# Performance work log

Measured on AMD Instinct MI355X. Metric: run time of the kernel, lower is better.

The kernel has to match this reference:

```python
import jax, jax.numpy as jnp
import numpy as np
from math import factorial, sqrt, pi

L = 10  # must match init_kwargs


def setup_inputs() -> dict:
    key = jax.random.key(0)
    pos = jax.random.normal(key, (2_000_000, 3), dtype=jnp.float32)
    return {"pos": pos}


def _cpow_tables(zr, zi, nmax):
    """Powers (zr + i*zi)^n for n=0..nmax. Returns (nmax+1, N) real and imag parts.
    Matches powcmplx in the source (repeated complex multiply), computed once."""
    reals = [jnp.ones_like(zr)]
    imags = [jnp.zeros_like(zr)]
    for _ in range(nmax):
        r, im = reals[-1], imags[-1]
        reals.append(zr * r - zi * im)
        imags.append(zr * im + zi * r)
    return jnp.stack(reals), jnp.stack(imags)


def reference(pos):
    norms = jnp.linalg.norm(pos, axis=1)            # (N,)
    mask = (norms > 0).astype(pos.dtype)            # replaces boolean indexing ids
    x, y, x0 = pos[:, 0], pos[:, 1], pos[:, 2]
    xpl1r, xpl1i = -0.5 * x, -0.5 * y
    xm1r, xm1i = 0.5 * x, -0.5 * y
    # precompute all needed complex powers (same math as powcmplx, deduplicated)
    z1r_t, z1i_t = _cpow_tables(xpl1r, xpl1i, L)    # (L+1, N)
    z2r_t, z2i_t = _cpow_tables(xm1r, xm1i, L)

    clms = [None] * ((L + 1) ** 2)
    i = 0
    for l in range(L + 1):
        rl = norms ** l
        for M in range(-l, 1):
            m = abs(M)
            shr = jnp.zeros_like(x)
            shi = jnp.zeros_like(x)
            for p in range(l + 1):
                q = p - m
                s = l - p - q
                if q >= 0 and s >= 0:
                    z1r, z1i = z1r_t[p], z1i_t[p]
                    z2r, z2i = z2r_t[q], z2i_t[q]
                    # NOTE: faithful to source, including its quirks:
                    # zreal uses z1r**2 - z2i**2, and the term is scaled by x0
                    # (x0**s is computed in the source but never used).
                    zreal = z1r ** 2 - z2i ** 2
                    zimag = z1r * z2i + z1i * z2r
                    c = 1.0 / (factorial(p) * factorial(q) * factorial(s))
                    shr = shr + zreal * x0 * c
                    shi = shi + zimag * x0 * c
            scale = sqrt(factorial(l + m) * factorial(l - m)) * sqrt((2 * l + 1) / (4.0 * pi))
            clm_r = jnp.sum(shr * rl * mask) * scale
            clm_i = jnp.sum(shi * rl * mask) * scale
            if m == 0:
                clms[i] = clm_r
            else:
                f = sqrt(2.0) * (-1) ** m
                clms[i] = f * clm_i
                clms[i + 2 * m] = f * clm_r
            i += 1
        i += l
    return jnp.stack(clms).reshape(-1, 1)  # ((L+1)^2, 1)
```

## Files before the change

### kernel.cpp

```cpp
#include <hip/hip_runtime.h>

namespace {

typedef float v2f __attribute__((ext_vector_type(2)));

constexpr int LMAX  = 10;
constexpr int NPART = 4;
constexpr int PART_OF_L[LMAX + 1] = {3, 2, 1, 0, 1, 2, 3, 3, 2, 1, 0};
constexpr double PI_D = 3.14159265358979323846;

constexpr double dfact(int n) {
    double r = 1.0;
    for (int i = 2; i <= n; ++i) r *= (double)i;
    return r;
}

constexpr double csqrt(double x) {
    if (x <= 0.0) return 0.0;
    double g = x > 1.0 ? x : 1.0;
    for (int i = 0; i < 100; ++i) g = 0.5 * (g + x / g);
    return g;
}

constexpr double FACT[LMAX + 1] = {1., 1., 2., 6., 24., 120., 720., 5040., 40320., 362880., 3628800.};

constexpr int NM_M = 66;
constexpr int mi(int p, int l) { return l * (l + 1) / 2 + p; }
constexpr int ni_base(int l) {
    int c = 0;
    for (int ll = 0; ll < l; ++ll) c += ll / 2;
    return c;
}
constexpr int ni(int q, int l) { return NM_M + ni_base(l) + (q - 1); }
constexpr int NM_N  = 25;
constexpr int NMOM  = NM_M + NM_N;
constexpr int ZSLOT = NMOM;
constexpr int WS_FLOATS = NMOM + 1;

constexpr int part_lmax(int part) {
    int mx = 0;
    for (int l = 0; l <= LMAX; ++l)
        if (PART_OF_L[l] == part) mx = l;
    return mx;
}
constexpr int nls(int part) {
    int c = 0;
    for (int l = 0; l <= LMAX; ++l)
        if (PART_OF_L[l] == part) ++c;
    return c;
}
constexpr int lidx(int part, int l) {
    int c = 0;
    for (int ll = 0; ll < l; ++ll)
        if (PART_OF_L[ll] == part) ++c;
    return c;
}
constexpr int part_ls(int part, int k) {
    int c = 0;
    for (int l = 0; l <= LMAX; ++l)
        if (PART_OF_L[l] == part) {
            if (c == k) return l;
            ++c;
        }
    return -1;
}
constexpr int nM(int part) {
    int c = 0;
    for (int l = 0; l <= LMAX; ++l)
        if (PART_OF_L[l] == part) c += l + 1;
    return c;
}
constexpr int nN(int part) {
    int c = 0;
    for (int l = 0; l <= LMAX; ++l)
        if (PART_OF_L[l] == part) c += l / 2;
    return c;
}
constexpr int nMom(int part) { return nM(part) + nN(part); }
constexpr int nI(int part) {
    int c = 0;
    for (int l = 0; l <= LMAX; ++l)
        if (PART_OF_L[l] == part) c += l;
    return c;
}
constexpr int nAcc(int part) { return nMom(part) + nI(part); }

constexpr int locM(int part, int p, int l) {
    int c = 0;
    for (int ll = 0; ll < l; ++ll)
        if (PART_OF_L[ll] == part) c += ll + 1;
    return c + p;
}
constexpr int locN(int part, int q, int l) {
    int c = nM(part);
    for (int ll = 0; ll < l; ++ll)
        if (PART_OF_L[ll] == part) c += ll / 2;
    return c + (q - 1);
}
constexpr int locI(int part, int m, int l) {
    int c = nMom(part);
    for (int ll = 0; ll < l; ++ll)
        if (PART_OF_L[ll] == part) c += ll;
    return c + (m - 1);
}

constexpr int MAXMOM = 25;
constexpr int MAXIMG = 15;

constexpr float ci_coef(int l, int m, int q) {
    const double c = 1.0 / (FACT[q + m] * FACT[q] * FACT[l - m - 2 * q]);
    return (q & 1) ? (float)(-c) : (float)c;
}

struct PartTab {
    short wsmap[NPART][MAXMOM];
    int   omap[NPART][MAXIMG];
    float oscl[NPART][MAXIMG];
};

constexpr PartTab make_pt() {
    PartTab t{};
    for (int part = 0; part < NPART; ++part) {
        for (int l = 0; l <= LMAX; ++l) {
            if (PART_OF_L[l] != part) continue;
            for (int p = 0; p <= l; ++p) t.wsmap[part][locM(part, p, l)] = (short)mi(p, l);
            for (int q = 1; q <= l / 2; ++q) t.wsmap[part][locN(part, q, l)] = (short)ni(q, l);
            for (int m = 1; m <= l; ++m) {
                const int    k     = locI(part, m, l) - nMom(part);
                const double scale = csqrt(dfact(l + m) * dfact(l - m)) * csqrt((2 * l + 1) / (4.0 * PI_D));
                const double f     = csqrt(2.0) * ((m & 1) ? -1.0 : 1.0);
                const double fold  = ((l - m) <= 1) ? 1.0 / (dfact(m) * dfact(l - m)) : 1.0;
                t.omap[part][k] = l * l + l - m;
                t.oscl[part][k] = (float)(f * scale * fold);
            }
        }
    }
    return t;
}

struct CombTab {
    int   out[66];
    float scale[66];
    int   nt[66];
    float c[66][6];
    short mIx[66][6];
    short nIx[66][6];
};

constexpr CombTab make_comb() {
    CombTab t{};
    int k = 0;
    for (int l = 0; l <= LMAX; ++l) {
        for (int m = 0; m <= l; ++m) {
            const double scale = csqrt(dfact(l + m) * dfact(l - m)) * csqrt((2 * l + 1) / (4.0 * PI_D));
            const double f     = (m == 0) ? 1.0 : csqrt(2.0) * ((m & 1) ? -1.0 : 1.0);
            t.out[k]   = (m == 0) ? l * l + l : l * l + l + m;
            t.scale[k] = (float)(f * scale);
            const int Q = (l - m) / 2;
            t.nt[k]     = Q + 1;
            for (int q = 0; q <= Q; ++q) {
                const double c = 1.0 / (FACT[q + m] * FACT[q] * FACT[l - m - 2 * q]);
                t.c[k][q]   = (float)c;
                t.mIx[k][q] = (short)mi(q + m, l);
                t.nIx[k][q] = (short)(q >= 1 ? ni(q, l) : ZSLOT);
            }
            ++k;
        }
    }
    return t;
}

__constant__ PartTab c_pt = make_pt();
__constant__ CombTab c_cb = make_comb();

__device__ __forceinline__ void pk_fma(v2f& d, v2f a, v2f b) {
    asm("v_pk_fma_f32 %0, %1, %2, %0" : "+v"(d) : "v"(a), "v"(b));
}

__device__ __forceinline__ void load_pair(const float* __restrict__ pos, int ip, int n,
                                          v2f& X, v2f& Y, v2f& Z) {
    const int i0 = 2 * ip;
    if (i0 + 1 < n) {
        const float2* p2 = reinterpret_cast<const float2*>(pos + 3 * i0);
        const float2  a = p2[0], b = p2[1], d = p2[2];
        X.x = a.x; X.y = b.y;
        Y.x = a.y; Y.y = d.x;
        Z.x = b.x; Z.y = d.y;
    } else if (i0 < n) {
        X.x = pos[3 * i0]; Y.x = pos[3 * i0 + 1]; Z.x = pos[3 * i0 + 2];
        X.y = 0.f; Y.y = 0.f; Z.y = 0.f;
    } else {
        X = (v2f)(0.f); Y = (v2f)(0.f); Z = (v2f)(0.f);
    }
}

}

template <int PART>
__device__ __forceinline__ void sht_part(const float* __restrict__ pos, float* __restrict__ out,
                                         float* __restrict__ ws, int n, int nblk) {
    constexpr int PL  = part_lmax(PART);
    constexpr int QX  = PL / 2;
    constexpr int NL  = nls(PART);
    constexpr int NMO = nMom(PART);
    constexpr int NAC = nAcc(PART);

    v2f acc[NAC];
#pragma unroll
    for (int k = 0; k < NAC; ++k) acc[k] = (v2f)(0.f);

    const int bid    = (int)(blockIdx.x >> 2);
    const int tid    = bid * 256 + (int)threadIdx.x;
    const int stride = nblk * 256;
    const int npair  = (n + 1) >> 1;

    v2f X, Y, Z;
    int ip = tid;
    load_pair(pos, ip, n, X, Y, Z);

    while (ip < npair) {
        const int inext = ip + stride;
        v2f       nX, nY, nZ;
        load_pair(pos, inext, n, nX, nY, nZ);

        const v2f r2 = X * X + Y * Y + Z * Z;
        v2f       nrm;
        nrm.x = sqrtf(r2.x);
        nrm.y = sqrtf(r2.y);
        v2f w0;
        w0.x = (nrm.x > 0.f) ? Z.x : 0.f;
        w0.y = (nrm.y > 0.f) ? Z.y : 0.f;

        const v2f ar  = -0.5f * X;
        const v2f ai  = -0.5f * Y;
        const v2f rho = ar * ar + ai * ai;

        v2f wl[NL];
        {
            const v2f p2v = nrm * nrm;
            const v2f p4v = p2v * p2v;
            const v2f p8v = p4v * p4v;
#pragma unroll
            for (int k = 0; k < NL; ++k) {
                const int l = part_ls(PART, k);
                v2f       t = w0;
                if (l & 1) t = t * nrm;
                if (l & 2) t = t * p2v;
                if (l & 4) t = t * p4v;
                if (l & 8) t = t * p8v;
                wl[k] = t;
            }
        }

        v2f zi[PL + 1];
        v2f zrc = (v2f)(1.f), zic = (v2f)(0.f);
#pragma unroll
        for (int p = 0; p <= PL; ++p) {
            if (p) {
                const v2f nr = ar * zrc - ai * zic;
                zic          = ar * zic + ai * zrc;
                zrc          = nr;
            }
            zi[p] = zic;
            const v2f srp = zrc * zrc;
#pragma unroll
            for (int l = 0; l <= LMAX; ++l)
                if (PART_OF_L[l] == PART && l >= p)
                    pk_fma(acc[locM(PART, p, l)], srp, wl[lidx(PART, l)]);
            if (p >= 1 && p <= QX) {
                const v2f sip = zic * zic;
#pragma unroll
                for (int l = 0; l <= LMAX; ++l)
                    if (PART_OF_L[l] == PART && l >= 2 * p)
                        pk_fma(acc[locN(PART, p, l)], sip, wl[lidx(PART, l)]);
            }
        }

#pragma unroll
        for (int l = 0; l <= LMAX; ++l) {
            if (PART_OF_L[l] != PART) continue;
            const v2f wrl = wl[lidx(PART, l)];
#pragma unroll
            for (int m = 1; m <= l; ++m) {
                const int Q = (l - m) >> 1;
                if (Q == 0) {
                    pk_fma(acc[locI(PART, m, l)], zi[m], wrl);
                } else {
                    v2f tq = (v2f)(ci_coef(l, m, Q));
#pragma unroll
                    for (int q = Q - 1; q >= 0; --q) tq = tq * rho + ci_coef(l, m, q);
                    pk_fma(acc[locI(PART, m, l)], tq * zi[m], wrl);
                }
            }
        }

        ip = inext;
        X  = nX;
        Y  = nY;
        Z  = nZ;
    }

    __shared__ float red[4][NAC];
    const int lane = threadIdx.x & 63;
    const int wav  = threadIdx.x >> 6;
#pragma unroll
    for (int k = 0; k < NAC; ++k) {
        float v = acc[k].x + acc[k].y;
#pragma unroll
        for (int off = 32; off > 0; off >>= 1) v += __shfl_down(v, off, 64);
        if (lane == 0) red[wav][k] = v;
    }
    __syncthreads();
    if ((int)threadIdx.x < NAC) {
        const int   k = (int)threadIdx.x;
        const float v = red[0][k] + red[1][k] + red[2][k] + red[3][k];
        if (k < NMO) {
            atomicAdd(&ws[c_pt.wsmap[PART][k]], v);
        } else {
            const int j = k - NMO;
            atomicAdd(&out[c_pt.omap[PART][j]], v * c_pt.oscl[PART][j]);
        }
    }
}

__global__ __launch_bounds__(256, 3) void sht_kernel(const float* __restrict__ pos,
                                                     float* __restrict__ out,
                                                     float* __restrict__ ws, int n, int nblk) {
    switch (blockIdx.x & 3) {
        case 0: sht_part<0>(pos, out, ws, n, nblk); break;
        case 1: sht_part<1>(pos, out, ws, n, nblk); break;
        case 2: sht_part<2>(pos, out, ws, n, nblk); break;
        default: sht_part<3>(pos, out, ws, n, nblk); break;
    }
}

__global__ void sht_combine(const float* __restrict__ ws, float* __restrict__ out) {
    const int t = (int)threadIdx.x;
    if (t < 66) {
        const int nt = c_cb.nt[t];
        float     v  = 0.f;
        for (int j = 0; j < nt; ++j)
            v += c_cb.c[t][j] * (ws[c_cb.mIx[t][j]] - ws[c_cb.nIx[t][j]]);
        out[c_cb.out[t]] = c_cb.scale[t] * v;
    }
}

extern "C" void kernel_launch(void* const* d_in, const int* in_sizes, int n_in,
                              void* d_out, int out_size, void* d_ws, size_t ws_size,
                              hipStream_t stream) {
    const float* pos = (const float*)d_in[0];
    float* out       = (float*)d_out;
    float* ws        = (float*)d_ws;
    const int n      = in_sizes[0] / 3;

    hipMemsetAsync(d_out, 0, (size_t)out_size * sizeof(float), stream);
    hipMemsetAsync(d_ws, 0, WS_FLOATS * sizeof(float), stream);

    const int threads = 256;
    const int nblk_per_part = 192;
    const int blocks        = NPART * nblk_per_part;
    sht_kernel<<<blocks, threads, 0, stream>>>(pos, out, ws, n, nblk_per_part);
    sht_combine<<<1, 128, 0, stream>>>(ws, out);
}
```

Before: 108.8 us.

## Fold combine kernel into main kernel via last-block ticket and force packed FP ops

```diff
diff --git a/kernel.cpp b/kernel.cpp
--- a/kernel.cpp
+++ b/kernel.cpp
@@ -32,10 +32,11 @@
     return c;
 }
 constexpr int ni(int q, int l) { return NM_M + ni_base(l) + (q - 1); }
-constexpr int NM_N  = 25;
-constexpr int NMOM  = NM_M + NM_N;
-constexpr int ZSLOT = NMOM;
-constexpr int WS_FLOATS = NMOM + 1;
+constexpr int NM_N   = 25;
+constexpr int NMOM   = NM_M + NM_N;
+constexpr int ZSLOT  = NMOM;
+constexpr int CSLOT  = NMOM + 1;
+constexpr int WS_FLOATS = NMOM + 2;
 
 constexpr int part_lmax(int part) {
     int mx = 0;
@@ -173,7 +174,17 @@
 __constant__ PartTab c_pt = make_pt();
 __constant__ CombTab c_cb = make_comb();
 
-__device__ __forceinline__ void pk_fma(v2f& d, v2f a, v2f b) {
+__device__ __forceinline__ v2f pk_mul(v2f a, v2f b) {
+    v2f d;
+    asm("v_pk_mul_f32 %0, %1, %2" : "=v"(d) : "v"(a), "v"(b));
+    return d;
+}
+__device__ __forceinline__ v2f pk_fma(v2f a, v2f b, v2f c) {
+    v2f d;
+    asm("v_pk_fma_f32 %0, %1, %2, %3" : "=v"(d) : "v"(a), "v"(b), "v"(c));
+    return d;
+}
+__device__ __forceinline__ void pk_acc(v2f& d, v2f a, v2f b) {
     asm("v_pk_fma_f32 %0, %1, %2, %0" : "+v"(d) : "v"(a), "v"(b));
 }
 
@@ -223,7 +234,7 @@
         v2f       nX, nY, nZ;
         load_pair(pos, inext, n, nX, nY, nZ);
 
-        const v2f r2 = X * X + Y * Y + Z * Z;
+        const v2f r2 = pk_fma(Z, Z, pk_fma(Y, Y, pk_mul(X, X)));
         v2f       nrm;
         nrm.x = sqrtf(r2.x);
         nrm.y = sqrtf(r2.y);
@@ -231,23 +242,27 @@
         w0.x = (nrm.x > 0.f) ? Z.x : 0.f;
         w0.y = (nrm.y > 0.f) ? Z.y : 0.f;
 
-        const v2f ar  = -0.5f * X;
-        const v2f ai  = -0.5f * Y;
-        const v2f rho = ar * ar + ai * ai;
+        const v2f half_neg = (v2f)(-0.5f);
+        const v2f ar  = pk_mul(half_neg, X);
+        const v2f ai  = pk_mul(half_neg, Y);
+        v2f       nai;
+        nai.x = -ai.x;
+        nai.y = -ai.y;
+        const v2f rho = pk_fma(ai, ai, pk_mul(ar, ar));
 
         v2f wl[NL];
         {
-            const v2f p2v = nrm * nrm;
-            const v2f p4v = p2v * p2v;
-            const v2f p8v = p4v * p4v;
+            const v2f p2v = pk_mul(nrm, nrm);
+            const v2f p4v = pk_mul(p2v, p2v);
+            const v2f p8v = pk_mul(p4v, p4v);
 #pragma unroll
             for (int k = 0; k < NL; ++k) {
                 const int l = part_ls(PART, k);
                 v2f       t = w0;
-                if (l & 1) t = t * nrm;
-                if (l & 2) t = t * p2v;
-                if (l & 4) t = t * p4v;
-                if (l & 8) t = t * p8v;
+                if (l & 1) t = pk_mul(t, nrm);
+                if (l & 2) t = pk_mul(t, p2v);
+                if (l & 4) t = pk_mul(t, p4v);
+                if (l & 8) t = pk_mul(t, p8v);
                 wl[k] = t;
             }
         }
@@ -257,22 +272,22 @@
 #pragma unroll
         for (int p = 0; p <= PL; ++p) {
             if (p) {
-                const v2f nr = ar * zrc - ai * zic;
-                zic          = ar * zic + ai * zrc;
+                const v2f nr = pk_fma(nai, zic, pk_mul(ar, zrc));
+                zic          = pk_fma(ai, zrc, pk_mul(ar, zic));
                 zrc          = nr;
             }
             zi[p] = zic;
-            const v2f srp = zrc * zrc;
+            const v2f srp = pk_mul(zrc, zrc);
 #pragma unroll
             for (int l = 0; l <= LMAX; ++l)
                 if (PART_OF_L[l] == PART && l >= p)
-                    pk_fma(acc[locM(PART, p, l)], srp, wl[lidx(PART, l)]);
+                    pk_acc(acc[locM(PART, p, l)], srp, wl[lidx(PART, l)]);
             if (p >= 1 && p <= QX) {
-                const v2f sip = zic * zic;
+                const v2f sip = pk_mul(zic, zic);
 #pragma unroll
                 for (int l = 0; l <= LMAX; ++l)
                     if (PART_OF_L[l] == PART && l >= 2 * p)
-                        pk_fma(acc[locN(PART, p, l)], sip, wl[lidx(PART, l)]);
+                        pk_acc(acc[locN(PART, p, l)], sip, wl[lidx(PART, l)]);
             }
         }
 
@@ -284,12 +299,12 @@
             for (int m = 1; m <= l; ++m) {
                 const int Q = (l - m) >> 1;
                 if (Q == 0) {
-                    pk_fma(acc[locI(PART, m, l)], zi[m], wrl);
+                    pk_acc(acc[locI(PART, m, l)], zi[m], wrl);
                 } else {
                     v2f tq = (v2f)(ci_coef(l, m, Q));
 #pragma unroll
                     for (int q = Q - 1; q >= 0; --q) tq = tq * rho + ci_coef(l, m, q);
-                    pk_fma(acc[locI(PART, m, l)], tq * zi[m], wrl);
+                    pk_acc(acc[locI(PART, m, l)], pk_mul(tq, zi[m]), wrl);
                 }
             }
         }
@@ -332,15 +347,24 @@
         case 2: sht_part<2>(pos, out, ws, n, nblk); break;
         default: sht_part<3>(pos, out, ws, n, nblk); break;
     }
-}
-
-__global__ void sht_combine(const float* __restrict__ ws, float* __restrict__ out) {
-    const int t = (int)threadIdx.x;
-    if (t < 66) {
+
+    __shared__ bool s_last;
+    __syncthreads();
+    if (threadIdx.x == 0) {
+        __threadfence();
+        const unsigned old = atomicAdd((unsigned*)&ws[CSLOT], 1u);
+        s_last = (old == (unsigned)(gridDim.x - 1));
+    }
+    __syncthreads();
+    if (s_last && (int)threadIdx.x < 66) {
+        const int t  = (int)threadIdx.x;
         const int nt = c_cb.nt[t];
         float     v  = 0.f;
-        for (int j = 0; j < nt; ++j)
-            v += c_cb.c[t][j] * (ws[c_cb.mIx[t][j]] - ws[c_cb.nIx[t][j]]);
+        for (int j = 0; j < nt; ++j) {
+            const float mv = atomicAdd(&ws[c_cb.mIx[t][j]], 0.f);
+            const float nv = atomicAdd(&ws[c_cb.nIx[t][j]], 0.f);
+            v += c_cb.c[t][j] * (mv - nv);
+        }
         out[c_cb.out[t]] = c_cb.scale[t] * v;
     }
 }
@@ -360,5 +384,4 @@
     const int nblk_per_part = 192;
     const int blocks        = NPART * nblk_per_part;
     sht_kernel<<<blocks, threads, 0, stream>>>(pos, out, ws, n, nblk_per_part);
-    sht_combine<<<1, 128, 0, stream>>>(ws, out);
-}
+}
```

After: 129.9 us. +19.4%, slower.
